# Kernel optimization log

Measured on AMD Instinct MI355X. Metric: run time of the kernel, lower is better.

The kernel has to match this reference:

```python
import jax, jax.numpy as jnp
import numpy as np

DIM = 192
HEADS = 6
HEAD_DIM = DIM // HEADS
K = 3          # kernel_size
PAD = 1
STRIDE = 2
SCALE = HEAD_DIM ** -0.5
B, H, W = 16, 56, 56


def setup_inputs() -> dict:
    key = jax.random.key(0)
    ks = jax.random.split(key, 6)
    x = jax.random.normal(ks[0], (B, H, W, DIM), jnp.float32)
    # Linear weights stored as [in, out] so y = x @ W + b (== torch x @ W.T)
    Wv = jax.random.normal(ks[1], (DIM, DIM), jnp.float32) * 0.05          # v_pj, no bias
    Wa = jax.random.normal(ks[2], (DIM, K**4 * HEADS), jnp.float32) * 0.05  # attn linear
    ba = jax.random.normal(ks[3], (K**4 * HEADS,), jnp.float32) * 0.01
    Wp = jax.random.normal(ks[4], (DIM, DIM), jnp.float32) * 0.05           # proj
    bp = jax.random.normal(ks[5], (DIM,), jnp.float32) * 0.01
    return {"x": x, "Wv": Wv, "Wa": Wa, "ba": ba, "Wp": Wp, "bp": bp}


def reference(x, Wv, Wa, ba, Wp, bp):
    # Dropout layers act as identity (eval mode).
    Bn, Hn, Wn, C = x.shape
    h = -(-Hn // STRIDE)  # ceil(H/stride) = 28
    w = -(-Wn // STRIDE)
    KK = K * K

    # --- value projection + unfold (im2col over K x K window, stride STRIDE) ---
    v = x @ Wv  # [B,H,W,C]
    vp = jnp.pad(v, ((0, 0), (PAD, PAD), (PAD, PAD), (0, 0)))
    # patches: [B,h,w,K*K,C]; loop is over the fixed 3x3 kernel taps only
    patches = jnp.stack(
        [vp[:, i:i + STRIDE * h:STRIDE, j:j + STRIDE * w:STRIDE, :]
         for i in range(K) for j in range(K)], axis=3)
    patches = patches.reshape(Bn, h * w, KK, HEADS, HEAD_DIM)

    # --- attention weights from avg-pooled map (H divisible by STRIDE here) ---
    pooled = x.reshape(Bn, h, STRIDE, w, STRIDE, C).mean(axis=(2, 4))  # [B,h,w,C]
    a = pooled.reshape(Bn, h * w, C) @ Wa + ba                         # [B,hw,K^4*heads]
    a = a.reshape(Bn, h * w, HEADS, KK, KK) * SCALE
    a = jax.nn.softmax(a, axis=-1)

    # --- windowed attention: [B,hw,heads,K2,K2] x [B,hw,K2,heads,hd] ---
    out = jnp.einsum('bnhpq,bnqhd->bnphd', a, patches)  # [B,hw,K2,heads,hd]
    out = out.reshape(Bn, h, w, KK, C)

    # --- fold (scatter-add of overlapping patches back to HxW) ---
    acc = jnp.zeros((Bn, Hn + 2 * PAD, Wn + 2 * PAD, C), x.dtype)
    idx = 0
    for i in range(K):
        for j in range(K):
            acc = acc.at[:, i:i + STRIDE * h:STRIDE, j:j + STRIDE * w:STRIDE, :].add(out[:, :, :, idx, :])
            idx += 1
    y = acc[:, PAD:PAD + Hn, PAD:PAD + Wn, :]

    return y @ Wp + bp
```

## Files before the change

### kernel.cpp

```cpp
#include <hip/hip_runtime.h>
#include <cstdint>
#include <cstddef>

#define DIMC    192
#define NHEADS  6
#define NATT    486
#define NB      16
#define NH      56
#define NWW     56
#define HPOOL   28
#define WPOOL   28
#define NPIX    784
#define VH      58
#define VW      58
#define MROWS   (NB*NH*NWW)
#define MPOOL   (NB*NPIX)
#define XELEMS  (MROWS*DIMC)
#define SCALE_A 0.17677669529663687f

using bf16x8 = __attribute__((ext_vector_type(8))) short;
using f32x4  = __attribute__((ext_vector_type(4))) float;

static __device__ __forceinline__ unsigned short f2bf(float f) {
    unsigned int u = __float_as_uint(f);
    unsigned int r = (u + 0x7fffu + ((u >> 16) & 1u)) >> 16;
    return (unsigned short)r;
}
static __device__ __forceinline__ float bf2f(unsigned short u) {
    return __uint_as_float((unsigned int)u << 16);
}

static __device__ __forceinline__ void gload_lds16(const void* src, void* lds) {
    __builtin_amdgcn_global_load_lds(
        (const __attribute__((address_space(1))) void*)src,
        (__attribute__((address_space(3))) void*)lds, 16, 0, 0);
}

__global__ __launch_bounds__(256)
void prep_kernel(const float* __restrict__ Wv, const float* __restrict__ Wp,
                 const float* __restrict__ Wa, const float* __restrict__ x,
                 unsigned short* __restrict__ WTv, unsigned short* __restrict__ WTp,
                 unsigned short* __restrict__ WaT, unsigned int* __restrict__ vpu,
                 unsigned short* __restrict__ xb)
{
    int idx = blockIdx.x * 256 + threadIdx.x;
    if (idx < 73728) {
        int sel = idx / 36864;
        int r   = idx - sel * 36864;
        int n   = r / DIMC;
        int k   = r - n * DIMC;
        const float* W = sel ? Wp : Wv;
        unsigned short* WT = sel ? WTp : WTv;
        WT[r] = f2bf(W[k * DIMC + n]);
    } else if (idx < 172032) {
        int r = idx - 73728;
        int n = r / DIMC;
        int k = r - n * DIMC;
        WaT[r] = (n < NATT) ? f2bf(Wa[(size_t)k * NATT + n] * SCALE_A) : (unsigned short)0;
    } else if (idx < 522240) {
        int i2   = idx - 172032;
        int cu   = i2 % 96;
        int rest = i2 / 96;
        int b    = rest / 228;
        int p    = rest - b * 228;
        int hi, wi;
        if (p < 58)       { hi = 0;  wi = p; }
        else if (p < 116) { hi = 57; wi = p - 58; }
        else { int q = p - 116; hi = 1 + (q >> 1); wi = (q & 1) * 57; }
        vpu[(((size_t)b * VH + hi) * VW + wi) * 96 + cu] = 0u;
    } else {
        size_t xi = (size_t)(idx - 522240) * 8;
        float4 v0 = *(const float4*)(x + xi);
        float4 v1 = *(const float4*)(x + xi + 4);
        bf16x8 u;
        u[0] = (short)f2bf(v0.x); u[1] = (short)f2bf(v0.y);
        u[2] = (short)f2bf(v0.z); u[3] = (short)f2bf(v0.w);
        u[4] = (short)f2bf(v1.x); u[5] = (short)f2bf(v1.y);
        u[6] = (short)f2bf(v1.z); u[7] = (short)f2bf(v1.w);
        *(bf16x8*)(xb + xi) = u;
    }
}

static __device__ __forceinline__
void stage_tile_async(const unsigned short* __restrict__ Ab, unsigned short* As, int t)
{
#pragma unroll
    for (int i = 0; i < 6; ++i) {
        int L     = i * 8192 + t * 16;
        int row   = L / 384;
        int inrow = L - row * 384;
        int s     = (row & 7) << 4;
        const unsigned short* src = Ab + (size_t)row * DIMC + ((inrow ^ s) >> 1);
        gload_lds16(src, (char*)As + i * 8192 + (t >> 6) * 1024);
    }
}

static __device__ __forceinline__
void gemm0_body(const unsigned short* __restrict__ xb, const unsigned short* __restrict__ WT,
                unsigned short* __restrict__ vp, int by, int t, char* smem)
{
    unsigned short* As = (unsigned short*)smem;

    const int l  = t & 63;
    const int w  = t >> 6;
    const int wr = w >> 1;
    const int wc = w & 1;

    stage_tile_async(xb + (size_t)by * 128 * DIMC, As, t);
    __syncthreads();

    f32x4 acc[2][6];
#pragma unroll
    for (int mi = 0; mi < 2; ++mi)
#pragma unroll
        for (int ni = 0; ni < 6; ++ni) acc[mi][ni] = (f32x4)0.f;

    const int arow0 = wr * 32 + (l & 15);
    const int kb    = (l >> 4) << 4;

#pragma unroll
    for (int ks = 0; ks < 6; ++ks) {
        bf16x8 a[2], b[6];
#pragma unroll
        for (int mi = 0; mi < 2; ++mi) {
            int row = arow0 + mi * 16;
            int off = (row * 384 + ks * 64 + kb) ^ ((row & 7) << 4);
            a[mi] = *(const bf16x8*)((const char*)As + off);
        }
#pragma unroll
        for (int ni = 0; ni < 6; ++ni) {
            int n = wc * 96 + ni * 16 + (l & 15);
            b[ni] = *(const bf16x8*)(WT + (size_t)n * DIMC + ks * 32 + ((l >> 4) << 3));
        }
#pragma unroll
        for (int mi = 0; mi < 2; ++mi)
#pragma unroll
            for (int ni = 0; ni < 6; ++ni)
                acc[mi][ni] = __builtin_amdgcn_mfma_f32_16x16x32_bf16(
                    a[mi], b[ni], acc[mi][ni], 0, 0, 0);
    }

    __syncthreads();
#pragma unroll
    for (int mi = 0; mi < 2; ++mi) {
#pragma unroll
        for (int r = 0; r < 4; ++r) {
            int row = wr * 32 + mi * 16 + ((l >> 4) << 2) + r;
#pragma unroll
            for (int ni = 0; ni < 6; ++ni) {
                int col = wc * 96 + ni * 16 + (l & 15);
                As[row * DIMC + col] = f2bf(acc[mi][ni][r]);
            }
        }
    }
    __syncthreads();
#pragma unroll
    for (int i = 0; i < 6; ++i) {
        int f   = i * 4096 + t * 8;
        int row = f / DIMC;
        int k   = f - row * DIMC;
        int m   = by * 128 + row;
        int bb  = m / (NH * NWW);
        int rr  = m - bb * (NH * NWW);
        int hi  = rr / NWW;
        int wi  = rr - hi * NWW;
        bf16x8 v = *(const bf16x8*)&As[f];
        unsigned short* dst = vp + (((size_t)bb * VH + hi + 1) * VW + (wi + 1)) * DIMC + k;
        *(bf16x8*)dst = v;
    }
}

static __device__ __forceinline__
void pool_body(const float* __restrict__ x, const unsigned short* __restrict__ WaT,
               const float* __restrict__ ba, unsigned short* __restrict__ attn,
               int by, int t, char* smem)
{
    unsigned short* As = (unsigned short*)smem;
    float (*Cs)[489]   = (float(*)[489])smem;
    float* ba_s        = (float*)(smem + 31296);

    const int l  = t & 63;
    const int w  = t >> 6;
    const int wr = w >> 2;
    const int wc = w & 3;

    if (t < NATT) ba_s[t] = ba[t] * SCALE_A;

#pragma unroll
    for (int i = 0; i < 6; ++i) {
        int f   = i * 2048 + t * 4;
        int row = f / DIMC;
        int k   = f - row * DIMC;
        int m   = by * 64 + row;
        int b   = m / NPIX;
        int r   = m - b * NPIX;
        int hh  = r / WPOOL;
        int ww  = r - hh * WPOOL;
        const float* xp = x + (((size_t)(b * NH + hh * 2)) * NWW + ww * 2) * DIMC + k;
        float4 v0 = *(const float4*)(xp);
        float4 v1 = *(const float4*)(xp + DIMC);
        float4 v2 = *(const float4*)(xp + (size_t)NWW * DIMC);
        float4 v3 = *(const float4*)(xp + (size_t)NWW * DIMC + DIMC);
        ushort4 u;
        u.x = f2bf(0.25f * (v0.x + v1.x + v2.x + v3.x));
        u.y = f2bf(0.25f * (v0.y + v1.y + v2.y + v3.y));
        u.z = f2bf(0.25f * (v0.z + v1.z + v2.z + v3.z));
        u.w = f2bf(0.25f * (v0.w + v1.w + v2.w + v3.w));
        int off = (row * 384 + k * 2) ^ ((row & 7) << 4);
        *(ushort4*)((char*)As + off) = u;
    }
    __syncthreads();

    f32x4 acc[2][8];
#pragma unroll
    for (int mi = 0; mi < 2; ++mi)
#pragma unroll
        for (int ni = 0; ni < 8; ++ni) acc[mi][ni] = (f32x4)0.f;

    const int arow0 = wr * 32 + (l & 15);
    const int kb    = (l >> 4) << 4;

#pragma unroll
    for (int ks = 0; ks < 6; ++ks) {
        bf16x8 a[2], b[8];
#pragma unroll
        for (int mi = 0; mi < 2; ++mi) {
            int row = arow0 + mi * 16;
            int off = (row * 384 + ks * 64 + kb) ^ ((row & 7) << 4);
            a[mi] = *(const bf16x8*)((const char*)As + off);
        }
#pragma unroll
        for (int ni = 0; ni < 8; ++ni) {
            int n = wc * 128 + ni * 16 + (l & 15);
            b[ni] = *(const bf16x8*)(WaT + (size_t)n * DIMC + ks * 32 + ((l >> 4) << 3));
        }
#pragma unroll
        for (int mi = 0; mi < 2; ++mi)
#pragma unroll
            for (int ni = 0; ni < 8; ++ni)
                acc[mi][ni] = __builtin_amdgcn_mfma_f32_16x16x32_bf16(
                    a[mi], b[ni], acc[mi][ni], 0, 0, 0);
    }

    __syncthreads();

#pragma unroll
    for (int r0 = 0; r0 < 64; r0 += 16) {
        const int mi = (r0 >> 4) & 1;
        if (wr == (r0 >> 5)) {
#pragma unroll
            for (int ni = 0; ni < 8; ++ni) {
                int col = wc * 128 + ni * 16 + (l & 15);
                if (col < NATT) {
#pragma unroll
                    for (int r = 0; r < 4; ++r)
                        Cs[((l >> 4) << 2) + r][col] =
                            (mi == 0 ? acc[0][ni][r] : acc[1][ni][r]) + ba_s[col];
                }
            }
        }
        __syncthreads();
        for (int g = t; g < 864; g += 512) {
            int lr = g / 54;
            int cg = g - lr * 54;
            const float* ap = &Cs[lr][cg * 9];
            float mx = ap[0];
#pragma unroll
            for (int q = 1; q < 9; ++q) mx = fmaxf(mx, ap[q]);
            float e[9];
            float sum = 0.f;
#pragma unroll
            for (int q = 0; q < 9; ++q) { e[q] = __expf(ap[q] - mx); sum += e[q]; }
            float inv = 1.f / sum;
            int m = by * 64 + r0 + lr;
            unsigned short* dst = attn + ((size_t)m * 54 + cg) * 16;
#pragma unroll
            for (int q = 0; q < 9; ++q) dst[q] = f2bf(e[q] * inv);
        }
        __syncthreads();
    }
}

__global__ __launch_bounds__(512)
void phase1_kernel(const unsigned short* __restrict__ xb, const float* __restrict__ x,
                   const unsigned short* __restrict__ WTv,
                   const unsigned short* __restrict__ WaT, const float* __restrict__ ba,
                   unsigned short* __restrict__ vp, unsigned short* __restrict__ attn)
{
    __shared__ __align__(16) char smem[49152];
    const int t = threadIdx.x;
    if (blockIdx.x < 392) gemm0_body(xb, WTv, vp, blockIdx.x, t, smem);
    else                  pool_body(x, WaT, ba, attn, blockIdx.x - 392, t, smem);
}

__global__ __launch_bounds__(512)
void gemm1_kernel(const unsigned short* __restrict__ Av, const unsigned short* __restrict__ WT,
                  const float* __restrict__ bias, float* __restrict__ Cv)
{
    __shared__ __align__(16) unsigned short As[128 * DIMC];

    const int t  = threadIdx.x;
    const int l  = t & 63;
    const int w  = t >> 6;
    const int wr = w >> 1;
    const int wc = w & 1;
    const int by = blockIdx.x;

    stage_tile_async(Av + (size_t)by * 128 * DIMC, As, t);
    __syncthreads();

    f32x4 acc[2][6];
#pragma unroll
    for (int mi = 0; mi < 2; ++mi)
#pragma unroll
        for (int ni = 0; ni < 6; ++ni) acc[mi][ni] = (f32x4)0.f;

    const int arow0 = wr * 32 + (l & 15);
    const int kb    = (l >> 4) << 4;

#pragma unroll
    for (int ks = 0; ks < 6; ++ks) {
        bf16x8 a[2], b[6];
#pragma unroll
        for (int mi = 0; mi < 2; ++mi) {
            int row = arow0 + mi * 16;
            int off = (row * 384 + ks * 64 + kb) ^ ((row & 7) << 4);
            a[mi] = *(const bf16x8*)((const char*)As + off);
        }
#pragma unroll
        for (int ni = 0; ni < 6; ++ni) {
            int n = wc * 96 + ni * 16 + (l & 15);
            b[ni] = *(const bf16x8*)(WT + (size_t)n * DIMC + ks * 32 + ((l >> 4) << 3));
        }
#pragma unroll
        for (int mi = 0; mi < 2; ++mi)
#pragma unroll
            for (int ni = 0; ni < 6; ++ni)
                acc[mi][ni] = __builtin_amdgcn_mfma_f32_16x16x32_bf16(
                    a[mi], b[ni], acc[mi][ni], 0, 0, 0);
    }

    float* fAs = (float*)As;
#pragma unroll
    for (int chunk = 0; chunk < 4; ++chunk) {
        __syncthreads();
        if (wr == chunk) {
#pragma unroll
            for (int mi = 0; mi < 2; ++mi) {
#pragma unroll
                for (int r = 0; r < 4; ++r) {
                    int rowl = mi * 16 + ((l >> 4) << 2) + r;
#pragma unroll
                    for (int ni = 0; ni < 6; ++ni) {
                        int col = wc * 96 + ni * 16 + (l & 15);
                        fAs[rowl * DIMC + col] = acc[mi][ni][r];
                    }
                }
            }
        }
        __syncthreads();
#pragma unroll
        for (int i = 0; i < 3; ++i) {
            int f   = i * 2048 + t * 4;
            int row = f / DIMC;
            int k   = f - row * DIMC;
            int m   = by * 128 + chunk * 32 + row;
            float4 v  = *(const float4*)&fAs[f];
            float4 bv = *(const float4*)&bias[k];
            v.x += bv.x; v.y += bv.y; v.z += bv.z; v.w += bv.w;
            *(float4*)(Cv + (size_t)m * DIMC + k) = v;
        }
    }
}

template<int NI, int NJ>
static __device__ __forceinline__ void gather_body(
    int b, int p, int qc, int head, int c,
    const unsigned short* __restrict__ attn, const unsigned short* __restrict__ vp,
    unsigned short* __restrict__ y)
{
    const int pr = p >> 1;
    const int qr = qc >> 1;

    bf16x8        aw8[NI * NJ];
    unsigned short aw9[NI * NJ];
    ushort2       v[NI * NJ][9];
    bool          ok[NI * NJ];

#pragma unroll
    for (int wi = 0; wi < NI; ++wi) {
        const bool hv  = (NI == 1) || (wi == 0) || (pr + 1 < HPOOL);
        const int  hhs = hv ? (pr + wi) : (HPOOL - 1);
        const int  iof = (NI == 1) ? 1 : (wi ? 0 : 2);
#pragma unroll
        for (int wj = 0; wj < NJ; ++wj) {
            const bool wv  = (NJ == 1) || (wj == 0) || (qr + 1 < WPOOL);
            const int  wws = wv ? (qr + wj) : (WPOOL - 1);
            const int  jof = (NJ == 1) ? 1 : (wj ? 0 : 2);
            const int  idx = wi * NJ + wj;
            ok[idx] = hv && wv;

            const unsigned short* ap = attn +
                ((size_t)((b * NPIX + hhs * WPOOL + wws) * 54 + head * 9 + iof * 3 + jof)) * 16;
            aw8[idx] = *(const bf16x8*)ap;
            aw9[idx] = ap[8];

            const unsigned short* vb = vp +
                (((size_t)(b * VH + 2 * hhs)) * VW + 2 * wws) * DIMC + c;
#pragma unroll
            for (int qi = 0; qi < 3; ++qi)
#pragma unroll
                for (int qj = 0; qj < 3; ++qj)
                    v[idx][qi * 3 + qj] = *(const ushort2*)(vb + ((size_t)qi * VW + qj) * DIMC);
        }
    }

    float accx = 0.f, accy = 0.f;
#pragma unroll
    for (int idx = 0; idx < NI * NJ; ++idx) {
#pragma unroll
        for (int k = 0; k < 9; ++k) {
            float a = ok[idx]
                ? ((k < 8) ? bf2f((unsigned short)aw8[idx][k]) : bf2f(aw9[idx]))
                : 0.f;
            accx = fmaf(a, bf2f(v[idx][k].x), accx);
            accy = fmaf(a, bf2f(v[idx][k].y), accy);
        }
    }

    size_t pix = (size_t)b * (NH * NWW) + (size_t)p * NWW + qc;
    ushort2 r;
    r.x = f2bf(accx);
    r.y = f2bf(accy);
    *(ushort2*)(y + pix * DIMC + c) = r;
}

__global__ __launch_bounds__(192)
void gather_kernel(const unsigned short* __restrict__ attn,
                   const unsigned short* __restrict__ vp,
                   unsigned short* __restrict__ y)
{
    const int t    = threadIdx.x;
    const int pl   = t / 96;
    const int c2   = t - pl * 96;
    const int c    = c2 * 2;
    const int head = c2 >> 4;

    const int flat = blockIdx.x;
    const int wgid = (flat & 7) * 3136 + (flat >> 3);
    const int b    = wgid / 1568;
    const int rr   = wgid - b * 1568;
    const int p    = rr / 28;
    const int wq   = rr - p * 28;
    const int qc   = wq + pl * 28;

    if (p & 1) {
        if (wq & 1) gather_body<2, 2>(b, p, qc, head, c, attn, vp, y);
        else        gather_body<2, 1>(b, p, qc, head, c, attn, vp, y);
    } else {
        if (wq & 1) gather_body<1, 2>(b, p, qc, head, c, attn, vp, y);
        else        gather_body<1, 1>(b, p, qc, head, c, attn, vp, y);
    }
}

extern "C" void kernel_launch(void* const* d_in, const int* in_sizes, int n_in,
                              void* d_out, int out_size, void* d_ws, size_t ws_size,
                              hipStream_t stream)
{
    const float* x  = (const float*)d_in[0];
    const float* Wv = (const float*)d_in[1];
    const float* Wa = (const float*)d_in[2];
    const float* ba = (const float*)d_in[3];
    const float* Wp = (const float*)d_in[4];
    const float* bp = (const float*)d_in[5];
    float* out = (float*)d_out;

    const size_t vp_elems   = (size_t)NB * VH * VW * DIMC;
    const size_t attn_elems = (size_t)MPOOL * 54 * 16;
    const size_t y_elems    = (size_t)MROWS * DIMC;

    unsigned short* vp   = (unsigned short*)d_ws;
    unsigned short* attn = vp + vp_elems;
    unsigned short* y    = attn + attn_elems;
    unsigned short* WTv  = y + y_elems;
    unsigned short* WTp  = WTv + 36864;
    unsigned short* WaT  = WTp + 36864;
    unsigned short* xb   = WaT + 98304;

    prep_kernel<<<6744, 256, 0, stream>>>(Wv, Wp, Wa, x, WTv, WTp, WaT,
                                          (unsigned int*)vp, xb);

    phase1_kernel<<<588, 512, 0, stream>>>(xb, x, WTv, WaT, ba, vp, attn);

    gather_kernel<<<25088, 192, 0, stream>>>(attn, vp, y);

    gemm1_kernel<<<MROWS / 128, 512, 0, stream>>>(y, WTp, bp, out);
}
```

Before: 115.9 us.

## Fuse fp32-to-bf16 conversion of x into the value-projection GEMM and shrink tiles

The prep kernel no longer converts the whole input to bf16 in a separate pass. The value GEMM now reads fp32 x directly, converts it into swizzled LDS, and stages its half of the weight matrix in LDS. Tiles shrink from 128x192 to 64x96, so the grid grows from 392 to 1568 GEMM blocks. The aim is to remove a full bf16 write and re-read of x and to spread the work across more blocks, at the cost of reading x twice across the two column halves and using more LDS per block. Softmax output stores are also vectorised.

```diff
diff --git a/kernel.cpp b/kernel.cpp
--- a/kernel.cpp
+++ b/kernel.cpp
@@ -15,7 +15,6 @@
 #define VW      58
 #define MROWS   (NB*NH*NWW)
 #define MPOOL   (NB*NPIX)
-#define XELEMS  (MROWS*DIMC)
 #define SCALE_A 0.17677669529663687f
 
 using bf16x8 = __attribute__((ext_vector_type(8))) short;
@@ -38,10 +37,9 @@
 
 __global__ __launch_bounds__(256)
 void prep_kernel(const float* __restrict__ Wv, const float* __restrict__ Wp,
-                 const float* __restrict__ Wa, const float* __restrict__ x,
+                 const float* __restrict__ Wa,
                  unsigned short* __restrict__ WTv, unsigned short* __restrict__ WTp,
-                 unsigned short* __restrict__ WaT, unsigned int* __restrict__ vpu,
-                 unsigned short* __restrict__ xb)
+                 unsigned short* __restrict__ WaT, unsigned int* __restrict__ vpu)
 {
     int idx = blockIdx.x * 256 + threadIdx.x;
     if (idx < 73728) {
@@ -57,7 +55,7 @@
         int n = r / DIMC;
         int k = r - n * DIMC;
         WaT[r] = (n < NATT) ? f2bf(Wa[(size_t)k * NATT + n] * SCALE_A) : (unsigned short)0;
-    } else if (idx < 522240) {
+    } else {
         int i2   = idx - 172032;
         int cu   = i2 % 96;
         int rest = i2 / 96;
@@ -68,105 +66,102 @@
         else if (p < 116) { hi = 57; wi = p - 58; }
         else { int q = p - 116; hi = 1 + (q >> 1); wi = (q & 1) * 57; }
         vpu[(((size_t)b * VH + hi) * VW + wi) * 96 + cu] = 0u;
-    } else {
-        size_t xi = (size_t)(idx - 522240) * 8;
-        float4 v0 = *(const float4*)(x + xi);
-        float4 v1 = *(const float4*)(x + xi + 4);
-        bf16x8 u;
-        u[0] = (short)f2bf(v0.x); u[1] = (short)f2bf(v0.y);
-        u[2] = (short)f2bf(v0.z); u[3] = (short)f2bf(v0.w);
-        u[4] = (short)f2bf(v1.x); u[5] = (short)f2bf(v1.y);
-        u[6] = (short)f2bf(v1.z); u[7] = (short)f2bf(v1.w);
-        *(bf16x8*)(xb + xi) = u;
     }
 }
 
 static __device__ __forceinline__
-void stage_tile_async(const unsigned short* __restrict__ Ab, unsigned short* As, int t)
-{
-#pragma unroll
-    for (int i = 0; i < 6; ++i) {
-        int L     = i * 8192 + t * 16;
-        int row   = L / 384;
-        int inrow = L - row * 384;
-        int s     = (row & 7) << 4;
-        const unsigned short* src = Ab + (size_t)row * DIMC + ((inrow ^ s) >> 1);
-        gload_lds16(src, (char*)As + i * 8192 + (t >> 6) * 1024);
-    }
-}
-
-static __device__ __forceinline__
-void gemm0_body(const unsigned short* __restrict__ xb, const unsigned short* __restrict__ WT,
-                unsigned short* __restrict__ vp, int by, int t, char* smem)
+void gemm0_body(const float* __restrict__ x, const unsigned short* __restrict__ WTv,
+                unsigned short* __restrict__ vp, int blk, int t, char* smem)
 {
     unsigned short* As = (unsigned short*)smem;
-
+    unsigned short* Ws = (unsigned short*)(smem + 24576);
+
+    const int tile = blk >> 1;
+    const int half = blk & 1;
     const int l  = t & 63;
     const int w  = t >> 6;
     const int wr = w >> 1;
     const int wc = w & 1;
 
-    stage_tile_async(xb + (size_t)by * 128 * DIMC, As, t);
-    __syncthreads();
-
-    f32x4 acc[2][6];
-#pragma unroll
-    for (int mi = 0; mi < 2; ++mi)
-#pragma unroll
-        for (int ni = 0; ni < 6; ++ni) acc[mi][ni] = (f32x4)0.f;
-
-    const int arow0 = wr * 32 + (l & 15);
-    const int kb    = (l >> 4) << 4;
-
-#pragma unroll
-    for (int ks = 0; ks < 6; ++ks) {
-        bf16x8 a[2], b[6];
-#pragma unroll
-        for (int mi = 0; mi < 2; ++mi) {
-            int row = arow0 + mi * 16;
-            int off = (row * 384 + ks * 64 + kb) ^ ((row & 7) << 4);
-            a[mi] = *(const bf16x8*)((const char*)As + off);
-        }
-#pragma unroll
-        for (int ni = 0; ni < 6; ++ni) {
-            int n = wc * 96 + ni * 16 + (l & 15);
-            b[ni] = *(const bf16x8*)(WT + (size_t)n * DIMC + ks * 32 + ((l >> 4) << 3));
-        }
-#pragma unroll
-        for (int mi = 0; mi < 2; ++mi)
-#pragma unroll
-            for (int ni = 0; ni < 6; ++ni)
-                acc[mi][ni] = __builtin_amdgcn_mfma_f32_16x16x32_bf16(
-                    a[mi], b[ni], acc[mi][ni], 0, 0, 0);
-    }
-
-    __syncthreads();
-#pragma unroll
-    for (int mi = 0; mi < 2; ++mi) {
-#pragma unroll
-        for (int r = 0; r < 4; ++r) {
-            int row = wr * 32 + mi * 16 + ((l >> 4) << 2) + r;
-#pragma unroll
-            for (int ni = 0; ni < 6; ++ni) {
-                int col = wc * 96 + ni * 16 + (l & 15);
-                As[row * DIMC + col] = f2bf(acc[mi][ni][r]);
-            }
-        }
-    }
-    __syncthreads();
+    const unsigned short* Wb = WTv + (size_t)half * 96 * DIMC;
+#pragma unroll
+    for (int i = 0; i < 5; ++i) {
+        int L = i * 8192 + t * 16;
+        if (L < 36864) {
+            int row   = L / 384;
+            int inrow = L - row * 384;
+            int s     = (row & 7) << 4;
+            const unsigned short* src = Wb + (size_t)row * DIMC + ((inrow ^ s) >> 1);
+            gload_lds16(src, (char*)Ws + (L & ~1023) + ((t & 63) << 4));
+        }
+    }
+
+    const float* Ab = x + (size_t)tile * 64 * DIMC;
 #pragma unroll
     for (int i = 0; i < 6; ++i) {
-        int f   = i * 4096 + t * 8;
+        int f   = i * 2048 + t * 4;
+        float4 v = *(const float4*)(Ab + f);
         int row = f / DIMC;
         int k   = f - row * DIMC;
-        int m   = by * 128 + row;
-        int bb  = m / (NH * NWW);
-        int rr  = m - bb * (NH * NWW);
-        int hi  = rr / NWW;
-        int wi  = rr - hi * NWW;
-        bf16x8 v = *(const bf16x8*)&As[f];
-        unsigned short* dst = vp + (((size_t)bb * VH + hi + 1) * VW + (wi + 1)) * DIMC + k;
-        *(bf16x8*)dst = v;
+        ushort4 u;
+        u.x = f2bf(v.x); u.y = f2bf(v.y); u.z = f2bf(v.z); u.w = f2bf(v.w);
+        int off = (row * 384 + k * 2) ^ ((row & 7) << 4);
+        *(ushort4*)((char*)As + off) = u;
+    }
+    __syncthreads();
+
+    f32x4 acc[3];
+#pragma unroll
+    for (int ni = 0; ni < 3; ++ni) acc[ni] = (f32x4)0.f;
+
+    const int arow = wr * 16 + (l & 15);
+    const int kb   = (l >> 4) << 4;
+    const int aswz = (arow & 7) << 4;
+
+#pragma unroll
+    for (int ks = 0; ks < 6; ++ks) {
+        bf16x8 a = *(const bf16x8*)((const char*)As +
+                        ((arow * 384 + ks * 64 + kb) ^ aswz));
+        bf16x8 b[3];
+#pragma unroll
+        for (int ni = 0; ni < 3; ++ni) {
+            int n = wc * 48 + ni * 16 + (l & 15);
+            b[ni] = *(const bf16x8*)((const char*)Ws +
+                        ((n * 384 + ks * 64 + kb) ^ ((n & 7) << 4)));
+        }
+#pragma unroll
+        for (int ni = 0; ni < 3; ++ni)
+            acc[ni] = __builtin_amdgcn_mfma_f32_16x16x32_bf16(a, b[ni], acc[ni], 0, 0, 0);
+    }
+
+    __syncthreads();
+    unsigned short* Cs = As;
+#pragma unroll
+    for (int ni = 0; ni < 3; ++ni) {
+        int col = wc * 48 + ni * 16 + (l & 15);
+#pragma unroll
+        for (int r = 0; r < 4; ++r) {
+            int row = wr * 16 + ((l >> 4) << 2) + r;
+            Cs[row * 96 + col] = f2bf(acc[ni][r]);
+        }
+    }
+    __syncthreads();
+#pragma unroll
+    for (int i = 0; i < 2; ++i) {
+        int idx = i * 8192 + t * 16;
+        if (idx < 12288) {
+            int row = idx / 192;
+            int cb  = idx - row * 192;
+            int m   = tile * 64 + row;
+            int bb  = m / (NH * NWW);
+            int rr  = m - bb * (NH * NWW);
+            int hi  = rr / NWW;
+            int wi  = rr - hi * NWW;
+            bf16x8 v = *(const bf16x8*)((const char*)Cs + idx);
+            unsigned short* dst = vp +
+                (((size_t)bb * VH + hi + 1) * VW + (wi + 1)) * DIMC + half * 96 + (cb >> 1);
+            *(bf16x8*)dst = v;
+        }
     }
 }
 
@@ -274,23 +269,39 @@
             float inv = 1.f / sum;
             int m = by * 64 + r0 + lr;
             unsigned short* dst = attn + ((size_t)m * 54 + cg) * 16;
-#pragma unroll
-            for (int q = 0; q < 9; ++q) dst[q] = f2bf(e[q] * inv);
+            bf16x8 ov;
+#pragma unroll
+            for (int q = 0; q < 8; ++q) ov[q] = (short)f2bf(e[q] * inv);
+            *(bf16x8*)dst = ov;
+            dst[8] = f2bf(e[8] * inv);
         }
         __syncthreads();
     }
 }
 
 __global__ __launch_bounds__(512)
-void phase1_kernel(const unsigned short* __restrict__ xb, const float* __restrict__ x,
-                   const unsigned short* __restrict__ WTv,
+void phase1_kernel(const float* __restrict__ x, const unsigned short* __restrict__ WTv,
                    const unsigned short* __restrict__ WaT, const float* __restrict__ ba,
                    unsigned short* __restrict__ vp, unsigned short* __restrict__ attn)
 {
-    __shared__ __align__(16) char smem[49152];
+    __shared__ __align__(16) char smem[61440];
     const int t = threadIdx.x;
-    if (blockIdx.x < 392) gemm0_body(xb, WTv, vp, blockIdx.x, t, smem);
-    else                  pool_body(x, WaT, ba, attn, blockIdx.x - 392, t, smem);
+    if (blockIdx.x < 1568) gemm0_body(x, WTv, vp, blockIdx.x, t, smem);
+    else                   pool_body(x, WaT, ba, attn, blockIdx.x - 1568, t, smem);
+}
+
+static __device__ __forceinline__
+void stage_tile_async(const unsigned short* __restrict__ Ab, unsigned short* As, int t)
+{
+#pragma unroll
+    for (int i = 0; i < 6; ++i) {
+        int L     = i * 8192 + t * 16;
+        int row   = L / 384;
+        int inrow = L - row * 384;
+        int s     = (row & 7) << 4;
+        const unsigned short* src = Ab + (size_t)row * DIMC + ((inrow ^ s) >> 1);
+        gload_lds16(src, (char*)As + i * 8192 + (t >> 6) * 1024);
+    }
 }
 
 __global__ __launch_bounds__(512)
@@ -485,12 +496,10 @@
     unsigned short* WTv  = y + y_elems;
     unsigned short* WTp  = WTv + 36864;
     unsigned short* WaT  = WTp + 36864;
-    unsigned short* xb   = WaT + 98304;
-
-    prep_kernel<<<6744, 256, 0, stream>>>(Wv, Wp, Wa, x, WTv, WTp, WaT,
-                                          (unsigned int*)vp, xb);
-
-    phase1_kernel<<<588, 512, 0, stream>>>(xb, x, WTv, WaT, ba, vp, attn);
+
+    prep_kernel<<<2040, 256, 0, stream>>>(Wv, Wp, Wa, WTv, WTp, WaT, (unsigned int*)vp);
+
+    phase1_kernel<<<1764, 512, 0, stream>>>(x, WTv, WaT, ba, vp, attn);
 
     gather_kernel<<<25088, 192, 0, stream>>>(attn, vp, y);
 
```

Measured after the change: 108.8 us. 6.1% less time.
